# Performance work log

Measured on AMD Instinct MI355X. Metric: run time of the kernel, lower is better.

## Reference

```python
import jax, jax.numpy as jnp
import numpy as np
import math

DIM = 512
N_HEADS = 8
N_KV_HEADS = 4
HEAD_DIM = DIM // N_HEADS
N_REP = N_HEADS // N_KV_HEADS


def setup_inputs() -> dict:
    key = jax.random.key(0)
    ks = jax.random.split(key, 6)
    B, S = 4, 8192
    x = jax.random.normal(ks[0], (B, S, DIM), dtype=jnp.float32)
    g = jnp.ones((DIM,), dtype=jnp.float32)
    sc = 1.0 / math.sqrt(DIM)
    wq = jax.random.normal(ks[1], (DIM, DIM), dtype=jnp.float32) * sc
    wk = jax.random.normal(ks[2], (N_KV_HEADS * HEAD_DIM, DIM), dtype=jnp.float32) * sc
    wv = jax.random.normal(ks[3], (N_KV_HEADS * HEAD_DIM, DIM), dtype=jnp.float32) * sc
    wo = jax.random.normal(ks[4], (DIM, DIM), dtype=jnp.float32) * sc
    return {"x": x, "g": g, "wq": wq, "wk": wk, "wv": wv, "wo": wo}


def _rmsnorm(x, g, eps=1e-6):
    var = jnp.mean(jnp.square(x), axis=-1, keepdims=True)
    return x * jax.lax.rsqrt(var + eps) * g


def _phi(x):
    # F.elu(x).clamp(min=-0.99) + 1
    return jnp.maximum(jax.nn.elu(x), -0.99) + 1.0


def reference(x, g, wq, wk, wv, wo):
    B, S, _ = x.shape
    h = _rmsnorm(x, g)
    scale = 1.0 / math.sqrt(HEAD_DIM)
    q = (h @ wq.T).reshape(B, S, N_HEADS, HEAD_DIM) * scale          # bshd
    k = (h @ wk.T).reshape(B, S, N_KV_HEADS, HEAD_DIM) * scale       # bsgd
    v = (h @ wv.T).reshape(B, S, N_KV_HEADS, HEAD_DIM)
    # GQA: repeat kv heads to n_heads
    k = jnp.repeat(k, N_REP, axis=2)  # (B,S,H,D)
    v = jnp.repeat(v, N_REP, axis=2)
    q = q.transpose(0, 2, 1, 3)  # (B,H,S,D)
    k = k.transpose(0, 2, 1, 3)
    v = v.transpose(0, 2, 1, 3)
    Q = _phi(q)
    K = _phi(k)
    KV = jnp.sum(K * v, axis=2)       # (B,H,D)  elementwise-product sum over s
    K_sum = jnp.sum(K, axis=2)        # (B,H,D)
    Z = jnp.einsum('bhsd,bhd->bhs', Q, K_sum)[..., None]  # (B,H,S,1)
    Y = Q * KV[:, :, None, :]         # (B,H,S,D)
    Y = Y / (Z + 1e-6)
    Y = Y.transpose(0, 2, 1, 3).reshape(B, S, N_HEADS * HEAD_DIM)
    return Y @ wo.T
```

## Files before the change

### kernel.cpp

```cpp
#include <hip/hip_runtime.h>
#include <math.h>

#define DIM 512
#define SEQ 8192
#define BATCH 4
#define RTOT (BATCH*SEQ)
#define SCALE 0.125f

typedef unsigned short ushort_t;
typedef __attribute__((ext_vector_type(8))) short short8;
typedef __attribute__((ext_vector_type(4))) float float4v;

#define AS1(p) ((__attribute__((address_space(1))) void*)(p))
#define AS3(p) ((__attribute__((address_space(3))) void*)(p))

__device__ __forceinline__ float phi_f(float x){
    return x > 0.f ? x + 1.f : fmaxf(expf(x), 0.01f);
}

__device__ __forceinline__ unsigned short f2bf(float f){
    unsigned int u = __float_as_uint(f);
    u += 0x7fffu + ((u >> 16) & 1u);
    return (unsigned short)(u >> 16);
}

#define WS_NEED 68689920ull

__global__ __launch_bounds__(256) void k_rmsh(const float* __restrict__ x, const float* __restrict__ g,
                                              float* __restrict__ wsf, ushort_t* __restrict__ hb){
    const int t = threadIdx.x, w = t>>6, L = t&63;
    const int row = blockIdx.x*4 + w;
    const float4* xr = (const float4*)(x + (size_t)row*DIM);
    float4 a = xr[L*2], c = xr[L*2+1];
    float s = a.x*a.x+a.y*a.y+a.z*a.z+a.w*a.w
            + c.x*c.x+c.y*c.y+c.z*c.z+c.w*c.w;
    #pragma unroll
    for(int off=1; off<64; off<<=1) s += __shfl_xor(s, off, 64);
    const float rf = rsqrtf(s*(1.0f/DIM) + 1e-6f);
    const float4* gr = (const float4*)g;
    float4 ga = gr[L*2], gb = gr[L*2+1];
    uint4 p;
    p.x = (unsigned)f2bf(a.x*ga.x*rf) | ((unsigned)f2bf(a.y*ga.y*rf)<<16);
    p.y = (unsigned)f2bf(a.z*ga.z*rf) | ((unsigned)f2bf(a.w*ga.w*rf)<<16);
    p.z = (unsigned)f2bf(c.x*gb.x*rf) | ((unsigned)f2bf(c.y*gb.y*rf)<<16);
    p.w = (unsigned)f2bf(c.z*gb.z*rf) | ((unsigned)f2bf(c.w*gb.w*rf)<<16);
    *(uint4*)(hb + (size_t)row*DIM + L*8) = p;
    if(blockIdx.x==0){
        for(int i=t;i<2048;i+=256) wsf[i]=0.f;
    }
}

__global__ __launch_bounds__(256) void k_wcast(const float* __restrict__ wq, const float* __restrict__ wk,
                                               const float* __restrict__ wv, const float* __restrict__ wo,
                                               ushort_t* __restrict__ wqb, ushort_t* __restrict__ wob,
                                               ushort_t* __restrict__ wkvb){
    const int idx = (blockIdx.x*256 + threadIdx.x)*4;
    const float* src; ushort_t* dst; int di;
    if(idx < 262144){ src = wq + idx; dst = wqb; di = idx; }
    else if(idx < 524288){ di = idx - 262144; src = wo + di; dst = wob; }
    else {
        int f = idx - 524288;
        int g = f >> 16, rem = f & 65535;
        int row = rem >> 9, col = rem & 511;
        src = (row < 64) ? (wk + (size_t)((g<<6)+row)*DIM + col)
                         : (wv + (size_t)((g<<6)+row-64)*DIM + col);
        dst = wkvb; di = f;
    }
    float4 v = *(const float4*)src;
    uint2 p;
    p.x = (unsigned)f2bf(v.x) | ((unsigned)f2bf(v.y)<<16);
    p.y = (unsigned)f2bf(v.z) | ((unsigned)f2bf(v.w)<<16);
    *(uint2*)(dst + di) = p;
}

__global__ __launch_bounds__(256) void k_kv_mfma(const ushort_t* __restrict__ hb,
                                                 const ushort_t* __restrict__ wkvb,
                                                 float* __restrict__ wsf){
    __shared__ ushort_t At[128*32];
    __shared__ ushort_t Bt[128*32];
    const int t = threadIdx.x, w = t>>6, L = t&63;
    const int lr = L&15, q = L>>4;
    const int r0 = blockIdx.x*128, gh = blockIdx.y;
    const int b = r0 >> 13;
    const int c0 = t, c1 = 256+t;
    const ushort_t* gA0 = hb + (size_t)(r0 + (c0>>2))*DIM + (c0&3)*8;
    const ushort_t* gA1 = hb + (size_t)(r0 + (c1>>2))*DIM + (c1&3)*8;
    const ushort_t* wb  = wkvb + (size_t)gh*128*DIM;
    const ushort_t* gB0 = wb + (size_t)(c0>>2)*DIM + (c0&3)*8;
    const ushort_t* gB1 = wb + (size_t)(c1>>2)*DIM + (c1&3)*8;

    float4v acc[2][8];
    #pragma unroll
    for(int i=0;i<2;i++)
        #pragma unroll
        for(int j=0;j<8;j++) acc[i][j] = (float4v){0.f,0.f,0.f,0.f};

    for(int ks=0; ks<16; ks++){
        __syncthreads();
        __builtin_amdgcn_global_load_lds(AS1(gA0), AS3(At + (w*64)*8),       16, 0, 0);
        __builtin_amdgcn_global_load_lds(AS1(gA1), AS3(At + (256 + w*64)*8), 16, 0, 0);
        __builtin_amdgcn_global_load_lds(AS1(gB0), AS3(Bt + (w*64)*8),       16, 0, 0);
        __builtin_amdgcn_global_load_lds(AS1(gB1), AS3(Bt + (256 + w*64)*8), 16, 0, 0);
        gA0 += 32; gA1 += 32; gB0 += 32; gB1 += 32;
        __syncthreads();
        short8 af[2], bf[8];
        #pragma unroll
        for(int mt=0; mt<2; mt++)
            af[mt] = *(const short8*)(At + (w*32 + mt*16 + lr)*32 + q*8);
        #pragma unroll
        for(int nt=0; nt<8; nt++)
            bf[nt] = *(const short8*)(Bt + (nt*16 + lr)*32 + q*8);
        #pragma unroll
        for(int mt=0; mt<2; mt++)
            #pragma unroll
            for(int nt=0; nt<8; nt++)
                acc[mt][nt] = __builtin_amdgcn_mfma_f32_16x16x32_bf16(af[mt], bf[nt], acc[mt][nt], 0,0,0);
    }

    #pragma unroll
    for(int nt=0; nt<4; nt++){
        float skv=0.f, sks=0.f;
        #pragma unroll
        for(int mt=0; mt<2; mt++)
            #pragma unroll
            for(int r=0; r<4; r++){
                float K = phi_f(acc[mt][nt][r]*SCALE);
                skv = fmaf(K, acc[mt][nt+4][r], skv);
                sks += K;
            }
        skv += __shfl_xor(skv,16,64); skv += __shfl_xor(skv,32,64);
        sks += __shfl_xor(sks,16,64); sks += __shfl_xor(sks,32,64);
        if(q==0){
            atomicAdd(&wsf[       b*256 + gh*64 + nt*16 + lr], skv);
            atomicAdd(&wsf[1024 + b*256 + gh*64 + nt*16 + lr], sks);
        }
    }
}

__global__ __launch_bounds__(256) void k_q_mfma(const ushort_t* __restrict__ hb,
                                                const ushort_t* __restrict__ wqb,
                                                const float* __restrict__ wsf,
                                                ushort_t* __restrict__ yb){
    __shared__ ushort_t At[128*32];
    __shared__ ushort_t Bt[128*32];
    __shared__ ushort_t Yt[128*128];
    const int t = threadIdx.x, w = t>>6, L = t&63;
    const int lr = L&15, q = L>>4;
    const int wr = w>>1, wc = w&1;
    const int r0 = blockIdx.x*128, ct = blockIdx.y;
    const int b = r0 >> 13;
    const int c0 = t, c1 = 256+t;
    const ushort_t* gA0 = hb + (size_t)(r0 + (c0>>2))*DIM + (c0&3)*8;
    const ushort_t* gA1 = hb + (size_t)(r0 + (c1>>2))*DIM + (c1&3)*8;
    const ushort_t* wbq = wqb + (size_t)ct*128*DIM;
    const ushort_t* gB0 = wbq + (size_t)(c0>>2)*DIM + (c0&3)*8;
    const ushort_t* gB1 = wbq + (size_t)(c1>>2)*DIM + (c1&3)*8;

    float4v acc[4][4];
    #pragma unroll
    for(int i=0;i<4;i++)
        #pragma unroll
        for(int j=0;j<4;j++) acc[i][j] = (float4v){0.f,0.f,0.f,0.f};

    for(int ks=0; ks<16; ks++){
        __syncthreads();
        __builtin_amdgcn_global_load_lds(AS1(gA0), AS3(At + (w*64)*8),       16, 0, 0);
        __builtin_amdgcn_global_load_lds(AS1(gA1), AS3(At + (256 + w*64)*8), 16, 0, 0);
        __builtin_amdgcn_global_load_lds(AS1(gB0), AS3(Bt + (w*64)*8),       16, 0, 0);
        __builtin_amdgcn_global_load_lds(AS1(gB1), AS3(Bt + (256 + w*64)*8), 16, 0, 0);
        gA0 += 32; gA1 += 32; gB0 += 32; gB1 += 32;
        __syncthreads();
        short8 af[4], bf[4];
        #pragma unroll
        for(int mt=0; mt<4; mt++)
            af[mt] = *(const short8*)(At + (wr*64 + mt*16 + lr)*32 + q*8);
        #pragma unroll
        for(int nt=0; nt<4; nt++)
            bf[nt] = *(const short8*)(Bt + (wc*64 + nt*16 + lr)*32 + q*8);
        #pragma unroll
        for(int mt=0; mt<4; mt++)
            #pragma unroll
            for(int nt=0; nt<4; nt++)
                acc[mt][nt] = __builtin_amdgcn_mfma_f32_16x16x32_bf16(af[mt], bf[nt], acc[mt][nt], 0,0,0);
    }

    float ksf[4], kvf[4];
    #pragma unroll
    for(int nt=0; nt<4; nt++){
        ksf[nt] = wsf[1024 + b*256 + ct*64 + nt*16 + lr];
        kvf[nt] = wsf[       b*256 + ct*64 + nt*16 + lr];
    }
    #pragma unroll
    for(int mt=0; mt<4; mt++)
        #pragma unroll
        for(int nt=0; nt<4; nt++)
            #pragma unroll
            for(int r=0; r<4; r++)
                acc[mt][nt][r] = phi_f(acc[mt][nt][r]*SCALE);
    float zi[4][4];
    #pragma unroll
    for(int mt=0; mt<4; mt++)
        #pragma unroll
        for(int r=0; r<4; r++){
            float zv = acc[mt][0][r]*ksf[0] + acc[mt][1][r]*ksf[1]
                     + acc[mt][2][r]*ksf[2] + acc[mt][3][r]*ksf[3];
            zv += __shfl_xor(zv,1,64); zv += __shfl_xor(zv,2,64);
            zv += __shfl_xor(zv,4,64); zv += __shfl_xor(zv,8,64);
            zi[mt][r] = 1.0f/(zv + 1e-6f);
        }
    #pragma unroll
    for(int mt=0; mt<4; mt++)
        #pragma unroll
        for(int nt=0; nt<4; nt++)
            #pragma unroll
            for(int r=0; r<4; r++)
                Yt[(wr*64 + mt*16 + q*4 + r)*128 + wc*64 + nt*16 + lr]
                    = f2bf(acc[mt][nt][r]*kvf[nt]*zi[mt][r]);
    __syncthreads();
    #pragma unroll
    for(int i=0;i<8;i++){
        int u = (i*256 + t)*8;
        int rr = u>>7, cc = u&127;
        *(uint4*)(yb + (size_t)(r0+rr)*DIM + ct*128 + cc) = *(const uint4*)(Yt + u);
    }
}

__global__ __launch_bounds__(256) void k_out_mfma(const ushort_t* __restrict__ yb,
                                                  const ushort_t* __restrict__ wob,
                                                  float* __restrict__ out){
    __shared__ ushort_t At[128*32];
    __shared__ ushort_t Bt[128*32];
    const int t = threadIdx.x, w = t>>6, L = t&63;
    const int lr = L&15, q = L>>4;
    const int wr = w>>1, wc = w&1;
    const int r0 = blockIdx.x*128, ct = blockIdx.y;
    const int c0 = t, c1 = 256+t;
    const ushort_t* gA0 = yb + (size_t)(r0 + (c0>>2))*DIM + (c0&3)*8;
    const ushort_t* gA1 = yb + (size_t)(r0 + (c1>>2))*DIM + (c1&3)*8;
    const ushort_t* wbo = wob + (size_t)ct*128*DIM;
    const ushort_t* gB0 = wbo + (size_t)(c0>>2)*DIM + (c0&3)*8;
    const ushort_t* gB1 = wbo + (size_t)(c1>>2)*DIM + (c1&3)*8;

    float4v acc[4][4];
    #pragma unroll
    for(int i=0;i<4;i++)
        #pragma unroll
        for(int j=0;j<4;j++) acc[i][j] = (float4v){0.f,0.f,0.f,0.f};

    for(int ks=0; ks<16; ks++){
        __syncthreads();
        __builtin_amdgcn_global_load_lds(AS1(gA0), AS3(At + (w*64)*8),       16, 0, 0);
        __builtin_amdgcn_global_load_lds(AS1(gA1), AS3(At + (256 + w*64)*8), 16, 0, 0);
        __builtin_amdgcn_global_load_lds(AS1(gB0), AS3(Bt + (w*64)*8),       16, 0, 0);
        __builtin_amdgcn_global_load_lds(AS1(gB1), AS3(Bt + (256 + w*64)*8), 16, 0, 0);
        gA0 += 32; gA1 += 32; gB0 += 32; gB1 += 32;
        __syncthreads();
        short8 af[4], bf[4];
        #pragma unroll
        for(int mt=0; mt<4; mt++)
            af[mt] = *(const short8*)(At + (wr*64 + mt*16 + lr)*32 + q*8);
        #pragma unroll
        for(int nt=0; nt<4; nt++)
            bf[nt] = *(const short8*)(Bt + (wc*64 + nt*16 + lr)*32 + q*8);
        #pragma unroll
        for(int mt=0; mt<4; mt++)
            #pragma unroll
            for(int nt=0; nt<4; nt++)
                acc[mt][nt] = __builtin_amdgcn_mfma_f32_16x16x32_bf16(af[mt], bf[nt], acc[mt][nt], 0,0,0);
    }
    #pragma unroll
    for(int mt=0; mt<4; mt++)
        #pragma unroll
        for(int nt=0; nt<4; nt++)
            #pragma unroll
            for(int r=0; r<4; r++)
                out[(size_t)(r0 + wr*64 + mt*16 + q*4 + r)*DIM + ct*128 + wc*64 + nt*16 + lr]
                    = acc[mt][nt][r];
}

#define OFF_KV 0
#define OFF_KS 1024
#define OFF_R  2048

__global__ __launch_bounds__(256) void k_rms_f32(const float* __restrict__ x, float* __restrict__ ws){
    const int row  = blockIdx.x*4 + (threadIdx.x>>6);
    const int lane = threadIdx.x & 63;
    const float4* xr = (const float4*)(x + (size_t)row*DIM);
    float4 a = xr[lane];
    float4 b = xr[lane+64];
    float s = a.x*a.x+a.y*a.y+a.z*a.z+a.w*a.w
            + b.x*b.x+b.y*b.y+b.z*b.z+b.w*b.w;
    #pragma unroll
    for(int off=32; off; off>>=1) s += __shfl_xor(s, off, 64);
    if(lane==0) ws[OFF_R+row] = rsqrtf(s*(1.0f/DIM) + 1e-6f);
    if(blockIdx.x==0){
        for(int i=threadIdx.x;i<2048;i+=256) ws[i]=0.f;
    }
}

__global__ __launch_bounds__(256) void k_kv_f32(const float* __restrict__ x, const float* __restrict__ g,
                                            const float* __restrict__ wk, const float* __restrict__ wv,
                                            float* __restrict__ ws){
    __shared__ float sAT[16][128];
    __shared__ float sB[16][128];
    __shared__ float rl[128];
    __shared__ float red[64][16];
    const int t  = threadIdx.x;
    const int r0 = blockIdx.x * 128;
    const int gh = blockIdx.y;
    const int b  = r0 / SEQ;
    if(t < 128) rl[t] = ws[OFF_R + r0 + t];
    const int ti = t & 15, tj = t >> 4;
    const int ri = ti*4, cj = tj*4;
    const int srow = t & 127;
    const int skk  = (t >> 7) * 8;
    const float* xrow = x + (size_t)(r0 + srow)*DIM + skk;
    const float* wrow = (srow < 64) ? (wk + (size_t)(gh*64 + srow)*DIM + skk)
                                    : (wv + (size_t)(gh*64 + (srow-64))*DIM + skk);
    const float* gp = g + skk;
    float accK[8][4], accV[8][4];
    #pragma unroll
    for(int i=0;i<8;i++)
        #pragma unroll
        for(int j=0;j<4;j++){ accK[i][j]=0.f; accV[i][j]=0.f; }
    __syncthreads();
    const float rr = rl[srow];
    for(int k0=0;k0<DIM;k0+=16){
        float4 xa = *(const float4*)(xrow + k0);
        float4 xb = *(const float4*)(xrow + k0 + 4);
        float4 ga = *(const float4*)(gp + k0);
        float4 gb = *(const float4*)(gp + k0 + 4);
        float4 wa = *(const float4*)(wrow + k0);
        float4 wb = *(const float4*)(wrow + k0 + 4);
        __syncthreads();
        sAT[skk+0][srow]=xa.x*ga.x*rr; sAT[skk+1][srow]=xa.y*ga.y*rr;
        sAT[skk+2][srow]=xa.z*ga.z*rr; sAT[skk+3][srow]=xa.w*ga.w*rr;
        sAT[skk+4][srow]=xb.x*gb.x*rr; sAT[skk+5][srow]=xb.y*gb.y*rr;
        sAT[skk+6][srow]=xb.z*gb.z*rr; sAT[skk+7][srow]=xb.w*gb.w*rr;
        sB[skk+0][srow]=wa.x; sB[skk+1][srow]=wa.y; sB[skk+2][srow]=wa.z; sB[skk+3][srow]=wa.w;
        sB[skk+4][srow]=wb.x; sB[skk+5][srow]=wb.y; sB[skk+6][srow]=wb.z; sB[skk+7][srow]=wb.w;
        __syncthreads();
        #pragma unroll
        for(int kk=0;kk<16;kk++){
            float4 a0 = *(const float4*)&sAT[kk][ri];
            float4 a1 = *(const float4*)&sAT[kk][ri+64];
            float4 bk = *(const float4*)&sB[kk][cj];
            float4 bv = *(const float4*)&sB[kk][cj+64];
            float av[8] = {a0.x,a0.y,a0.z,a0.w,a1.x,a1.y,a1.z,a1.w};
            float bk4[4]= {bk.x,bk.y,bk.z,bk.w};
            float bv4[4]= {bv.x,bv.y,bv.z,bv.w};
            #pragma unroll
            for(int i=0;i<8;i++)
                #pragma unroll
                for(int j=0;j<4;j++){
                    accK[i][j] = fmaf(av[i], bk4[j], accK[i][j]);
                    accV[i][j] = fmaf(av[i], bv4[j], accV[i][j]);
                }
        }
    }
    float pKV[4], pKs[4];
    #pragma unroll
    for(int j=0;j<4;j++){
        float skv=0.f, sks=0.f;
        #pragma unroll
        for(int i=0;i<8;i++){
            float kvv = phi_f(accK[i][j]*SCALE);
            skv = fmaf(kvv, accV[i][j], skv);
            sks += kvv;
        }
        pKV[j]=skv; pKs[j]=sks;
    }
    __syncthreads();
    #pragma unroll
    for(int j=0;j<4;j++) red[cj+j][ti] = pKV[j];
    __syncthreads();
    if(t<64){
        float s2=0.f;
        for(int i=0;i<16;i++) s2 += red[t][i];
        atomicAdd(&ws[OFF_KV + b*256 + gh*64 + t], s2);
    }
    __syncthreads();
    #pragma unroll
    for(int j=0;j<4;j++) red[cj+j][ti] = pKs[j];
    __syncthreads();
    if(t<64){
        float s2=0.f;
        for(int i=0;i<16;i++) s2 += red[t][i];
        atomicAdd(&ws[OFF_KS + b*256 + gh*64 + t], s2);
    }
}

__global__ __launch_bounds__(256) void k_qo_f32(const float* __restrict__ x, const float* __restrict__ g,
                                            const float* __restrict__ wq, const float* __restrict__ wo,
                                            const float* __restrict__ ws, float* __restrict__ out){
    __shared__ float qT[512][32];
    __shared__ float sAT[16][32];
    __shared__ float sB[16][128];
    __shared__ float rl[32];
    __shared__ float KVl[256];
    __shared__ float Ksl[256];
    __shared__ float zb[256];
    const int t  = threadIdx.x;
    const int r0 = blockIdx.x * 32;
    const int b  = r0 / SEQ;
    if(t<32) rl[t] = ws[OFF_R + r0 + t];
    KVl[t] = ws[OFF_KV + b*256 + t];
    Ksl[t] = ws[OFF_KS + b*256 + t];
    const int ti = t & 7, tj = t >> 3;
    const int ri = ti*4, cj = tj*4;
    const int srow = t & 31, skk = (t>>5)*2;
    const int sj = t & 127, skkB = (t>>7)*8;
    const float* xrow = x + (size_t)(r0+srow)*DIM + skk;
    const float* gp = g + skk;
    __syncthreads();
    const float rr = rl[srow];
    for(int ct=0; ct<4; ct++){
        const float* wqb = wq + (size_t)(ct*128 + sj)*DIM + skkB;
        float acc[4][4];
        #pragma unroll
        for(int i=0;i<4;i++)
            #pragma unroll
            for(int j=0;j<4;j++) acc[i][j]=0.f;
        for(int k0=0;k0<DIM;k0+=16){
            float2 xa = *(const float2*)(xrow + k0);
            float2 ga = *(const float2*)(gp + k0);
            float4 wa = *(const float4*)(wqb + k0);
            float4 wb2= *(const float4*)(wqb + k0 + 4);
            __syncthreads();
            sAT[skk+0][srow] = xa.x*ga.x*rr;
            sAT[skk+1][srow] = xa.y*ga.y*rr;
            sB[skkB+0][sj]=wa.x; sB[skkB+1][sj]=wa.y; sB[skkB+2][sj]=wa.z; sB[skkB+3][sj]=wa.w;
            sB[skkB+4][sj]=wb2.x; sB[skkB+5][sj]=wb2.y; sB[skkB+6][sj]=wb2.z; sB[skkB+7][sj]=wb2.w;
            __syncthreads();
            #pragma unroll
            for(int kk=0;kk<16;kk++){
                float4 a = *(const float4*)&sAT[kk][ri];
                float4 bb= *(const float4*)&sB[kk][cj];
                float av[4]={a.x,a.y,a.z,a.w};
                float bv[4]={bb.x,bb.y,bb.z,bb.w};
                #pragma unroll
                for(int i=0;i<4;i++)
                    #pragma unroll
                    for(int j=0;j<4;j++)
                        acc[i][j] = fmaf(av[i], bv[j], acc[i][j]);
            }
        }
        #pragma unroll
        for(int i=0;i<4;i++)
            #pragma unroll
            for(int j=0;j<4;j++)
                qT[ct*128+cj+j][ri+i] = phi_f(acc[i][j]*SCALE);
    }
    __syncthreads();
    {
        const int row = t>>3, h = t&7;
        const float* ks = &Ksl[(h>>1)*64];
        float z = 0.f;
        #pragma unroll
        for(int d=0;d<64;d++) z = fmaf(qT[h*64+d][row], ks[d], z);
        zb[row*8+h] = 1.0f/(z + 1e-6f);
    }
    __syncthreads();
    #pragma unroll 4
    for(int i2=0;i2<64;i2++){
        int f = i2*256 + t;
        int col = f>>5, row = f&31;
        int h = col>>6;
        float kvv = KVl[((h>>1)<<6) + (col&63)];
        qT[col][row] *= kvv * zb[row*8+h];
    }
    __syncthreads();
    for(int ct=0;ct<4;ct++){
        const float* wob = wo + (size_t)(ct*128 + sj)*DIM + skkB;
        float acc[4][4];
        #pragma unroll
        for(int i=0;i<4;i++)
            #pragma unroll
            for(int j=0;j<4;j++) acc[i][j]=0.f;
        for(int k0=0;k0<DIM;k0+=16){
            float4 wa = *(const float4*)(wob + k0);
            float4 wb2= *(const float4*)(wob + k0 + 4);
            __syncthreads();
            sB[skkB+0][sj]=wa.x; sB[skkB+1][sj]=wa.y; sB[skkB+2][sj]=wa.z; sB[skkB+3][sj]=wa.w;
            sB[skkB+4][sj]=wb2.x; sB[skkB+5][sj]=wb2.y; sB[skkB+6][sj]=wb2.z; sB[skkB+7][sj]=wb2.w;
            __syncthreads();
            #pragma unroll
            for(int kk=0;kk<16;kk++){
                float4 a = *(const float4*)&qT[k0+kk][ri];
                float4 bb= *(const float4*)&sB[kk][cj];
                float av[4]={a.x,a.y,a.z,a.w};
                float bv[4]={bb.x,bb.y,bb.z,bb.w};
                #pragma unroll
                for(int i=0;i<4;i++)
                    #pragma unroll
                    for(int j=0;j<4;j++)
                        acc[i][j] = fmaf(av[i], bv[j], acc[i][j]);
            }
        }
        #pragma unroll
        for(int i=0;i<4;i++){
            float4 st; st.x=acc[i][0]; st.y=acc[i][1]; st.z=acc[i][2]; st.w=acc[i][3];
            *(float4*)(out + (size_t)(r0+ri+i)*DIM + ct*128 + cj) = st;
        }
    }
}

extern "C" void kernel_launch(void* const* d_in, const int* in_sizes, int n_in,
                              void* d_out, int out_size, void* d_ws, size_t ws_size,
                              hipStream_t stream){
    (void)in_sizes; (void)n_in; (void)out_size;
    const float* x  = (const float*)d_in[0];
    const float* g  = (const float*)d_in[1];
    const float* wq = (const float*)d_in[2];
    const float* wk = (const float*)d_in[3];
    const float* wv = (const float*)d_in[4];
    const float* wo = (const float*)d_in[5];
    float* out = (float*)d_out;

    if(ws_size >= WS_NEED){
        float* wsf = (float*)d_ws;
        ushort_t* wqb  = (ushort_t*)((char*)d_ws + 8192);
        ushort_t* wob  = wqb  + 262144;
        ushort_t* wkvb = wob  + 262144;
        ushort_t* hb   = wkvb + 262144;
        ushort_t* yb   = hb   + 16777216;

        hipLaunchKernelGGL(k_rmsh,    dim3(RTOT/4),      dim3(256), 0, stream, x, g, wsf, hb);
        hipLaunchKernelGGL(k_wcast,   dim3(768),         dim3(256), 0, stream, wq, wk, wv, wo, wqb, wob, wkvb);
        hipLaunchKernelGGL(k_kv_mfma, dim3(RTOT/128, 4), dim3(256), 0, stream, hb, wkvb, wsf);
        hipLaunchKernelGGL(k_q_mfma,  dim3(RTOT/128, 4), dim3(256), 0, stream, hb, wqb, wsf, yb);
        hipLaunchKernelGGL(k_out_mfma,dim3(RTOT/128, 4), dim3(256), 0, stream, yb, wob, out);
    } else {
        float* ws = (float*)d_ws;
        hipLaunchKernelGGL(k_rms_f32, dim3(RTOT/4),      dim3(256), 0, stream, x, ws);
        hipLaunchKernelGGL(k_kv_f32,  dim3(RTOT/128, 4), dim3(256), 0, stream, x, g, wk, wv, ws);
        hipLaunchKernelGGL(k_qo_f32,  dim3(RTOT/32),     dim3(256), 0, stream, x, g, wq, wo, ws, out);
    }
}
```

Before: 228.7 us.

## Register-prefetch GEMM tiles two steps ahead and alias LDS in q kernel

Replaces the synchronous global_load_lds staging in the three MFMA GEMM kernels with register-staged loads issued two k-steps ahead, so global latency overlaps the MFMA work. Tiles are written to LDS after each compute step, and the loops are fully unrolled. The q kernel reuses the A/B staging LDS for the Y output tile to shrink its shared memory footprint, and launch bounds now request 2 blocks per SM. The cost is higher register pressure from the extra staging registers plus an occupancy hint that may force spills.

```diff
diff --git a/kernel.cpp b/kernel.cpp
--- a/kernel.cpp
+++ b/kernel.cpp
@@ -10,9 +10,6 @@
 typedef unsigned short ushort_t;
 typedef __attribute__((ext_vector_type(8))) short short8;
 typedef __attribute__((ext_vector_type(4))) float float4v;
-
-#define AS1(p) ((__attribute__((address_space(1))) void*)(p))
-#define AS3(p) ((__attribute__((address_space(3))) void*)(p))
 
 __device__ __forceinline__ float phi_f(float x){
     return x > 0.f ? x + 1.f : fmaxf(expf(x), 0.01f);
@@ -73,9 +70,9 @@
     *(uint2*)(dst + di) = p;
 }
 
-__global__ __launch_bounds__(256) void k_kv_mfma(const ushort_t* __restrict__ hb,
-                                                 const ushort_t* __restrict__ wkvb,
-                                                 float* __restrict__ wsf){
+__global__ __launch_bounds__(256,2) void k_kv_mfma(const ushort_t* __restrict__ hb,
+                                                   const ushort_t* __restrict__ wkvb,
+                                                   float* __restrict__ wsf){
     __shared__ ushort_t At[128*32];
     __shared__ ushort_t Bt[128*32];
     const int t = threadIdx.x, w = t>>6, L = t&63;
@@ -95,14 +92,22 @@
         #pragma unroll
         for(int j=0;j<8;j++) acc[i][j] = (float4v){0.f,0.f,0.f,0.f};
 
+    uint4 sa0[2], sa1[2], sb0[2], sb1[2];
+    sa0[1]=*(const uint4*)gA0; sa1[1]=*(const uint4*)gA1;
+    sb0[1]=*(const uint4*)gB0; sb1[1]=*(const uint4*)gB1;
+    *(uint4*)(At+c0*8)=sa0[1]; *(uint4*)(At+c1*8)=sa1[1];
+    *(uint4*)(Bt+c0*8)=sb0[1]; *(uint4*)(Bt+c1*8)=sb1[1];
+    sa0[0]=*(const uint4*)(gA0+32); sa1[0]=*(const uint4*)(gA1+32);
+    sb0[0]=*(const uint4*)(gB0+32); sb1[0]=*(const uint4*)(gB1+32);
+    __syncthreads();
+
+    #pragma unroll
     for(int ks=0; ks<16; ks++){
-        __syncthreads();
-        __builtin_amdgcn_global_load_lds(AS1(gA0), AS3(At + (w*64)*8),       16, 0, 0);
-        __builtin_amdgcn_global_load_lds(AS1(gA1), AS3(At + (256 + w*64)*8), 16, 0, 0);
-        __builtin_amdgcn_global_load_lds(AS1(gB0), AS3(Bt + (w*64)*8),       16, 0, 0);
-        __builtin_amdgcn_global_load_lds(AS1(gB1), AS3(Bt + (256 + w*64)*8), 16, 0, 0);
-        gA0 += 32; gA1 += 32; gB0 += 32; gB1 += 32;
-        __syncthreads();
+        const int pf = (ks+1)&1, wr_ = ks&1;
+        if(ks<14){
+            sa0[pf]=*(const uint4*)(gA0+(ks+2)*32); sa1[pf]=*(const uint4*)(gA1+(ks+2)*32);
+            sb0[pf]=*(const uint4*)(gB0+(ks+2)*32); sb1[pf]=*(const uint4*)(gB1+(ks+2)*32);
+        }
         short8 af[2], bf[8];
         #pragma unroll
         for(int mt=0; mt<2; mt++)
@@ -115,6 +120,12 @@
             #pragma unroll
             for(int nt=0; nt<8; nt++)
                 acc[mt][nt] = __builtin_amdgcn_mfma_f32_16x16x32_bf16(af[mt], bf[nt], acc[mt][nt], 0,0,0);
+        __syncthreads();
+        if(ks<15){
+            *(uint4*)(At+c0*8)=sa0[wr_]; *(uint4*)(At+c1*8)=sa1[wr_];
+            *(uint4*)(Bt+c0*8)=sb0[wr_]; *(uint4*)(Bt+c1*8)=sb1[wr_];
+            __syncthreads();
+        }
     }
 
     #pragma unroll
@@ -137,13 +148,13 @@
     }
 }
 
-__global__ __launch_bounds__(256) void k_q_mfma(const ushort_t* __restrict__ hb,
-                                                const ushort_t* __restrict__ wqb,
-                                                const float* __restrict__ wsf,
-                                                ushort_t* __restrict__ yb){
-    __shared__ ushort_t At[128*32];
-    __shared__ ushort_t Bt[128*32];
-    __shared__ ushort_t Yt[128*128];
+__global__ __launch_bounds__(256,2) void k_q_mfma(const ushort_t* __restrict__ hb,
+                                                  const ushort_t* __restrict__ wqb,
+                                                  const float* __restrict__ wsf,
+                                                  ushort_t* __restrict__ yb){
+    __shared__ ushort_t smem[128*128];
+    ushort_t* At = smem;
+    ushort_t* Bt = smem + 4096;
     const int t = threadIdx.x, w = t>>6, L = t&63;
     const int lr = L&15, q = L>>4;
     const int wr = w>>1, wc = w&1;
@@ -162,14 +173,22 @@
         #pragma unroll
         for(int j=0;j<4;j++) acc[i][j] = (float4v){0.f,0.f,0.f,0.f};
 
+    uint4 sa0[2], sa1[2], sb0[2], sb1[2];
+    sa0[1]=*(const uint4*)gA0; sa1[1]=*(const uint4*)gA1;
+    sb0[1]=*(const uint4*)gB0; sb1[1]=*(const uint4*)gB1;
+    *(uint4*)(At+c0*8)=sa0[1]; *(uint4*)(At+c1*8)=sa1[1];
+    *(uint4*)(Bt+c0*8)=sb0[1]; *(uint4*)(Bt+c1*8)=sb1[1];
+    sa0[0]=*(const uint4*)(gA0+32); sa1[0]=*(const uint4*)(gA1+32);
+    sb0[0]=*(const uint4*)(gB0+32); sb1[0]=*(const uint4*)(gB1+32);
+    __syncthreads();
+
+    #pragma unroll
     for(int ks=0; ks<16; ks++){
-        __syncthreads();
-        __builtin_amdgcn_global_load_lds(AS1(gA0), AS3(At + (w*64)*8),       16, 0, 0);
-        __builtin_amdgcn_global_load_lds(AS1(gA1), AS3(At + (256 + w*64)*8), 16, 0, 0);
-        __builtin_amdgcn_global_load_lds(AS1(gB0), AS3(Bt + (w*64)*8),       16, 0, 0);
-        __builtin_amdgcn_global_load_lds(AS1(gB1), AS3(Bt + (256 + w*64)*8), 16, 0, 0);
-        gA0 += 32; gA1 += 32; gB0 += 32; gB1 += 32;
-        __syncthreads();
+        const int pf = (ks+1)&1, wr_ = ks&1;
+        if(ks<14){
+            sa0[pf]=*(const uint4*)(gA0+(ks+2)*32); sa1[pf]=*(const uint4*)(gA1+(ks+2)*32);
+            sb0[pf]=*(const uint4*)(gB0+(ks+2)*32); sb1[pf]=*(const uint4*)(gB1+(ks+2)*32);
+        }
         short8 af[4], bf[4];
         #pragma unroll
         for(int mt=0; mt<4; mt++)
@@ -182,6 +201,12 @@
             #pragma unroll
             for(int nt=0; nt<4; nt++)
                 acc[mt][nt] = __builtin_amdgcn_mfma_f32_16x16x32_bf16(af[mt], bf[nt], acc[mt][nt], 0,0,0);
+        __syncthreads();
+        if(ks<15){
+            *(uint4*)(At+c0*8)=sa0[wr_]; *(uint4*)(At+c1*8)=sa1[wr_];
+            *(uint4*)(Bt+c0*8)=sb0[wr_]; *(uint4*)(Bt+c1*8)=sb1[wr_];
+            __syncthreads();
+        }
     }
 
     float ksf[4], kvf[4];
@@ -208,6 +233,7 @@
             zv += __shfl_xor(zv,4,64); zv += __shfl_xor(zv,8,64);
             zi[mt][r] = 1.0f/(zv + 1e-6f);
         }
+    ushort_t* Yt = smem;
     #pragma unroll
     for(int mt=0; mt<4; mt++)
         #pragma unroll
@@ -225,9 +251,9 @@
     }
 }
 
-__global__ __launch_bounds__(256) void k_out_mfma(const ushort_t* __restrict__ yb,
-                                                  const ushort_t* __restrict__ wob,
-                                                  float* __restrict__ out){
+__global__ __launch_bounds__(256,2) void k_out_mfma(const ushort_t* __restrict__ yb,
+                                                    const ushort_t* __restrict__ wob,
+                                                    float* __restrict__ out){
     __shared__ ushort_t At[128*32];
     __shared__ ushort_t Bt[128*32];
     const int t = threadIdx.x, w = t>>6, L = t&63;
@@ -247,14 +273,22 @@
         #pragma unroll
         for(int j=0;j<4;j++) acc[i][j] = (float4v){0.f,0.f,0.f,0.f};
 
+    uint4 sa0[2], sa1[2], sb0[2], sb1[2];
+    sa0[1]=*(const uint4*)gA0; sa1[1]=*(const uint4*)gA1;
+    sb0[1]=*(const uint4*)gB0; sb1[1]=*(const uint4*)gB1;
+    *(uint4*)(At+c0*8)=sa0[1]; *(uint4*)(At+c1*8)=sa1[1];
+    *(uint4*)(Bt+c0*8)=sb0[1]; *(uint4*)(Bt+c1*8)=sb1[1];
+    sa0[0]=*(const uint4*)(gA0+32); sa1[0]=*(const uint4*)(gA1+32);
+    sb0[0]=*(const uint4*)(gB0+32); sb1[0]=*(const uint4*)(gB1+32);
+    __syncthreads();
+
+    #pragma unroll
     for(int ks=0; ks<16; ks++){
-        __syncthreads();
-        __builtin_amdgcn_global_load_lds(AS1(gA0), AS3(At + (w*64)*8),       16, 0, 0);
-        __builtin_amdgcn_global_load_lds(AS1(gA1), AS3(At + (256 + w*64)*8), 16, 0, 0);
-        __builtin_amdgcn_global_load_lds(AS1(gB0), AS3(Bt + (w*64)*8),       16, 0, 0);
-        __builtin_amdgcn_global_load_lds(AS1(gB1), AS3(Bt + (256 + w*64)*8), 16, 0, 0);
-        gA0 += 32; gA1 += 32; gB0 += 32; gB1 += 32;
-        __syncthreads();
+        const int pf = (ks+1)&1, wr_ = ks&1;
+        if(ks<14){
+            sa0[pf]=*(const uint4*)(gA0+(ks+2)*32); sa1[pf]=*(const uint4*)(gA1+(ks+2)*32);
+            sb0[pf]=*(const uint4*)(gB0+(ks+2)*32); sb1[pf]=*(const uint4*)(gB1+(ks+2)*32);
+        }
         short8 af[4], bf[4];
         #pragma unroll
         for(int mt=0; mt<4; mt++)
@@ -267,6 +301,12 @@
             #pragma unroll
             for(int nt=0; nt<4; nt++)
                 acc[mt][nt] = __builtin_amdgcn_mfma_f32_16x16x32_bf16(af[mt], bf[nt], acc[mt][nt], 0,0,0);
+        __syncthreads();
+        if(ks<15){
+            *(uint4*)(At+c0*8)=sa0[wr_]; *(uint4*)(At+c1*8)=sa1[wr_];
+            *(uint4*)(Bt+c0*8)=sb0[wr_]; *(uint4*)(Bt+c1*8)=sb1[wr_];
+            __syncthreads();
+        }
     }
     #pragma unroll
     for(int mt=0; mt<4; mt++)
```

After: 408.7 us. +78.7%, slower.

## Fuse Q projection, linear attention and output GEMM into one row-block kernel

Applied to the files above, without the earlier changes.

Merges the Q GEMM, phi/normalisation epilogue and output projection into a single kernel that keeps the 64-row h tile and the bf16 Y tile in shared memory, so the Y intermediate is no longer written to and read back from global memory. The KV kernel is restructured the same way: the full 64x512 A tile is staged once into LDS, and weight fragments are read directly from global memory per wave instead of being double-synchronised into LDS each k-step. This cuts global traffic and barriers and shrinks workspace, at the cost of large per-thread accumulator arrays (4x8 tiles), 64KB LDS per block and uncached direct weight loads. Occupancy is limited by the launch bound of two blocks.

```diff
diff --git a/kernel.cpp b/kernel.cpp
--- a/kernel.cpp
+++ b/kernel.cpp
@@ -11,9 +11,6 @@
 typedef __attribute__((ext_vector_type(8))) short short8;
 typedef __attribute__((ext_vector_type(4))) float float4v;
 
-#define AS1(p) ((__attribute__((address_space(1))) void*)(p))
-#define AS3(p) ((__attribute__((address_space(3))) void*)(p))
-
 __device__ __forceinline__ float phi_f(float x){
     return x > 0.f ? x + 1.f : fmaxf(expf(x), 0.01f);
 }
@@ -24,7 +21,7 @@
     return (unsigned short)(u >> 16);
 }
 
-#define WS_NEED 68689920ull
+#define WS_NEED 35135488ull
 
 __global__ __launch_bounds__(256) void k_rmsh(const float* __restrict__ x, const float* __restrict__ g,
                                               float* __restrict__ wsf, ushort_t* __restrict__ hb){
@@ -73,47 +70,52 @@
     *(uint2*)(dst + di) = p;
 }
 
-__global__ __launch_bounds__(256) void k_kv_mfma(const ushort_t* __restrict__ hb,
-                                                 const ushort_t* __restrict__ wkvb,
-                                                 float* __restrict__ wsf){
-    __shared__ ushort_t At[128*32];
-    __shared__ ushort_t Bt[128*32];
+__device__ __forceinline__ void stage_A(const ushort_t* __restrict__ src, size_t r0,
+                                        ushort_t* As, int w, int L){
+    #pragma unroll
+    for(int i=0;i<16;i++){
+        const int row = i*4 + w;
+        uint4 v = *(const uint4*)(src + (size_t)(r0+row)*DIM + L*8);
+        *(uint4*)(&As[(L>>2)*2048 + row*32 + (L&3)*8]) = v;
+    }
+}
+
+__global__ __launch_bounds__(256,2) void k_kv2(const ushort_t* __restrict__ hb,
+                                               const ushort_t* __restrict__ wkvb,
+                                               float* __restrict__ wsf){
+    __shared__ ushort_t As[32768];
     const int t = threadIdx.x, w = t>>6, L = t&63;
     const int lr = L&15, q = L>>4;
-    const int r0 = blockIdx.x*128, gh = blockIdx.y;
-    const int b = r0 >> 13;
-    const int c0 = t, c1 = 256+t;
-    const ushort_t* gA0 = hb + (size_t)(r0 + (c0>>2))*DIM + (c0&3)*8;
-    const ushort_t* gA1 = hb + (size_t)(r0 + (c1>>2))*DIM + (c1&3)*8;
-    const ushort_t* wb  = wkvb + (size_t)gh*128*DIM;
-    const ushort_t* gB0 = wb + (size_t)(c0>>2)*DIM + (c0&3)*8;
-    const ushort_t* gB1 = wb + (size_t)(c1>>2)*DIM + (c1&3)*8;
-
-    float4v acc[2][8];
-    #pragma unroll
-    for(int i=0;i<2;i++)
+    const size_t r0 = (size_t)blockIdx.x*64;
+    const int b = (int)(r0 >> 13);
+
+    stage_A(hb, r0, As, w, L);
+    __syncthreads();
+
+    const ushort_t* bp[8];
+    #pragma unroll
+    for(int nt=0;nt<8;nt++)
+        bp[nt] = wkvb + ((size_t)w*128 + nt*16 + lr)*DIM + q*8;
+
+    float4v acc[4][8];
+    #pragma unroll
+    for(int i=0;i<4;i++)
         #pragma unroll
         for(int j=0;j<8;j++) acc[i][j] = (float4v){0.f,0.f,0.f,0.f};
 
+    #pragma unroll
     for(int ks=0; ks<16; ks++){
-        __syncthreads();
-        __builtin_amdgcn_global_load_lds(AS1(gA0), AS3(At + (w*64)*8),       16, 0, 0);
-        __builtin_amdgcn_global_load_lds(AS1(gA1), AS3(At + (256 + w*64)*8), 16, 0, 0);
-        __builtin_amdgcn_global_load_lds(AS1(gB0), AS3(Bt + (w*64)*8),       16, 0, 0);
-        __builtin_amdgcn_global_load_lds(AS1(gB1), AS3(Bt + (256 + w*64)*8), 16, 0, 0);
-        gA0 += 32; gA1 += 32; gB0 += 32; gB1 += 32;
-        __syncthreads();
-        short8 af[2], bf[8];
-        #pragma unroll
-        for(int mt=0; mt<2; mt++)
-            af[mt] = *(const short8*)(At + (w*32 + mt*16 + lr)*32 + q*8);
-        #pragma unroll
-        for(int nt=0; nt<8; nt++)
-            bf[nt] = *(const short8*)(Bt + (nt*16 + lr)*32 + q*8);
-        #pragma unroll
-        for(int mt=0; mt<2; mt++)
-            #pragma unroll
-            for(int nt=0; nt<8; nt++)
+        short8 bf[8];
+        #pragma unroll
+        for(int nt=0;nt<8;nt++) bf[nt] = *(const short8*)(bp[nt] + ks*32);
+        short8 af[4];
+        #pragma unroll
+        for(int mt=0;mt<4;mt++)
+            af[mt] = *(const short8*)(As + ks*2048 + (mt*16+lr)*32 + q*8);
+        #pragma unroll
+        for(int mt=0;mt<4;mt++)
+            #pragma unroll
+            for(int nt=0;nt<8;nt++)
                 acc[mt][nt] = __builtin_amdgcn_mfma_f32_16x16x32_bf16(af[mt], bf[nt], acc[mt][nt], 0,0,0);
     }
 
@@ -121,7 +123,7 @@
     for(int nt=0; nt<4; nt++){
         float skv=0.f, sks=0.f;
         #pragma unroll
-        for(int mt=0; mt<2; mt++)
+        for(int mt=0; mt<4; mt++)
             #pragma unroll
             for(int r=0; r<4; r++){
                 float K = phi_f(acc[mt][nt][r]*SCALE);
@@ -131,151 +133,129 @@
         skv += __shfl_xor(skv,16,64); skv += __shfl_xor(skv,32,64);
         sks += __shfl_xor(sks,16,64); sks += __shfl_xor(sks,32,64);
         if(q==0){
-            atomicAdd(&wsf[       b*256 + gh*64 + nt*16 + lr], skv);
-            atomicAdd(&wsf[1024 + b*256 + gh*64 + nt*16 + lr], sks);
-        }
-    }
-}
-
-__global__ __launch_bounds__(256) void k_q_mfma(const ushort_t* __restrict__ hb,
+            atomicAdd(&wsf[       b*256 + w*64 + nt*16 + lr], skv);
+            atomicAdd(&wsf[1024 + b*256 + w*64 + nt*16 + lr], sks);
+        }
+    }
+}
+
+__global__ __launch_bounds__(256,2) void k_qout(const ushort_t* __restrict__ hb,
                                                 const ushort_t* __restrict__ wqb,
+                                                const ushort_t* __restrict__ wob,
                                                 const float* __restrict__ wsf,
-                                                ushort_t* __restrict__ yb){
-    __shared__ ushort_t At[128*32];
-    __shared__ ushort_t Bt[128*32];
-    __shared__ ushort_t Yt[128*128];
+                                                float* __restrict__ out){
+    __shared__ ushort_t As[32768];
     const int t = threadIdx.x, w = t>>6, L = t&63;
     const int lr = L&15, q = L>>4;
-    const int wr = w>>1, wc = w&1;
-    const int r0 = blockIdx.x*128, ct = blockIdx.y;
-    const int b = r0 >> 13;
-    const int c0 = t, c1 = 256+t;
-    const ushort_t* gA0 = hb + (size_t)(r0 + (c0>>2))*DIM + (c0&3)*8;
-    const ushort_t* gA1 = hb + (size_t)(r0 + (c1>>2))*DIM + (c1&3)*8;
-    const ushort_t* wbq = wqb + (size_t)ct*128*DIM;
-    const ushort_t* gB0 = wbq + (size_t)(c0>>2)*DIM + (c0&3)*8;
-    const ushort_t* gB1 = wbq + (size_t)(c1>>2)*DIM + (c1&3)*8;
-
-    float4v acc[4][4];
+    const size_t r0 = (size_t)blockIdx.x*64;
+    const int b = (int)(r0 >> 13);
+
+    stage_A(hb, r0, As, w, L);
+    __syncthreads();
+
+    float4v acc[4][8];
     #pragma unroll
     for(int i=0;i<4;i++)
         #pragma unroll
-        for(int j=0;j<4;j++) acc[i][j] = (float4v){0.f,0.f,0.f,0.f};
-
-    for(int ks=0; ks<16; ks++){
-        __syncthreads();
-        __builtin_amdgcn_global_load_lds(AS1(gA0), AS3(At + (w*64)*8),       16, 0, 0);
-        __builtin_amdgcn_global_load_lds(AS1(gA1), AS3(At + (256 + w*64)*8), 16, 0, 0);
-        __builtin_amdgcn_global_load_lds(AS1(gB0), AS3(Bt + (w*64)*8),       16, 0, 0);
-        __builtin_amdgcn_global_load_lds(AS1(gB1), AS3(Bt + (256 + w*64)*8), 16, 0, 0);
-        gA0 += 32; gA1 += 32; gB0 += 32; gB1 += 32;
-        __syncthreads();
-        short8 af[4], bf[4];
-        #pragma unroll
-        for(int mt=0; mt<4; mt++)
-            af[mt] = *(const short8*)(At + (wr*64 + mt*16 + lr)*32 + q*8);
-        #pragma unroll
-        for(int nt=0; nt<4; nt++)
-            bf[nt] = *(const short8*)(Bt + (wc*64 + nt*16 + lr)*32 + q*8);
-        #pragma unroll
-        for(int mt=0; mt<4; mt++)
-            #pragma unroll
-            for(int nt=0; nt<4; nt++)
-                acc[mt][nt] = __builtin_amdgcn_mfma_f32_16x16x32_bf16(af[mt], bf[nt], acc[mt][nt], 0,0,0);
-    }
-
-    float ksf[4], kvf[4];
-    #pragma unroll
-    for(int nt=0; nt<4; nt++){
-        ksf[nt] = wsf[1024 + b*256 + ct*64 + nt*16 + lr];
-        kvf[nt] = wsf[       b*256 + ct*64 + nt*16 + lr];
-    }
-    #pragma unroll
-    for(int mt=0; mt<4; mt++)
-        #pragma unroll
-        for(int nt=0; nt<4; nt++)
-            #pragma unroll
-            for(int r=0; r<4; r++)
+        for(int j=0;j<8;j++) acc[i][j] = (float4v){0.f,0.f,0.f,0.f};
+
+    {
+        const ushort_t* bp[8];
+        #pragma unroll
+        for(int nt=0;nt<8;nt++)
+            bp[nt] = wqb + ((size_t)w*128 + nt*16 + lr)*DIM + q*8;
+        #pragma unroll
+        for(int ks=0; ks<16; ks++){
+            short8 bf[8];
+            #pragma unroll
+            for(int nt=0;nt<8;nt++) bf[nt] = *(const short8*)(bp[nt] + ks*32);
+            short8 af[4];
+            #pragma unroll
+            for(int mt=0;mt<4;mt++)
+                af[mt] = *(const short8*)(As + ks*2048 + (mt*16+lr)*32 + q*8);
+            #pragma unroll
+            for(int mt=0;mt<4;mt++)
+                #pragma unroll
+                for(int nt=0;nt<8;nt++)
+                    acc[mt][nt] = __builtin_amdgcn_mfma_f32_16x16x32_bf16(af[mt], bf[nt], acc[mt][nt], 0,0,0);
+        }
+    }
+
+    float ksf[8], kvf[8];
+    #pragma unroll
+    for(int nt=0;nt<8;nt++){
+        const int d = (nt&3)*16 + lr;
+        kvf[nt] = wsf[       b*256 + w*64 + d];
+        ksf[nt] = wsf[1024 + b*256 + w*64 + d];
+    }
+    #pragma unroll
+    for(int mt=0;mt<4;mt++)
+        #pragma unroll
+        for(int nt=0;nt<8;nt++)
+            #pragma unroll
+            for(int r=0;r<4;r++)
                 acc[mt][nt][r] = phi_f(acc[mt][nt][r]*SCALE);
-    float zi[4][4];
-    #pragma unroll
-    for(int mt=0; mt<4; mt++)
-        #pragma unroll
-        for(int r=0; r<4; r++){
-            float zv = acc[mt][0][r]*ksf[0] + acc[mt][1][r]*ksf[1]
+    float zi0[4][4], zi1[4][4];
+    #pragma unroll
+    for(int mt=0;mt<4;mt++)
+        #pragma unroll
+        for(int r=0;r<4;r++){
+            float z0 = acc[mt][0][r]*ksf[0] + acc[mt][1][r]*ksf[1]
                      + acc[mt][2][r]*ksf[2] + acc[mt][3][r]*ksf[3];
-            zv += __shfl_xor(zv,1,64); zv += __shfl_xor(zv,2,64);
-            zv += __shfl_xor(zv,4,64); zv += __shfl_xor(zv,8,64);
-            zi[mt][r] = 1.0f/(zv + 1e-6f);
-        }
-    #pragma unroll
-    for(int mt=0; mt<4; mt++)
-        #pragma unroll
-        for(int nt=0; nt<4; nt++)
-            #pragma unroll
-            for(int r=0; r<4; r++)
-                Yt[(wr*64 + mt*16 + q*4 + r)*128 + wc*64 + nt*16 + lr]
-                    = f2bf(acc[mt][nt][r]*kvf[nt]*zi[mt][r]);
-    __syncthreads();
-    #pragma unroll
-    for(int i=0;i<8;i++){
-        int u = (i*256 + t)*8;
-        int rr = u>>7, cc = u&127;
-        *(uint4*)(yb + (size_t)(r0+rr)*DIM + ct*128 + cc) = *(const uint4*)(Yt + u);
-    }
-}
-
-__global__ __launch_bounds__(256) void k_out_mfma(const ushort_t* __restrict__ yb,
-                                                  const ushort_t* __restrict__ wob,
-                                                  float* __restrict__ out){
-    __shared__ ushort_t At[128*32];
-    __shared__ ushort_t Bt[128*32];
-    const int t = threadIdx.x, w = t>>6, L = t&63;
-    const int lr = L&15, q = L>>4;
-    const int wr = w>>1, wc = w&1;
-    const int r0 = blockIdx.x*128, ct = blockIdx.y;
-    const int c0 = t, c1 = 256+t;
-    const ushort_t* gA0 = yb + (size_t)(r0 + (c0>>2))*DIM + (c0&3)*8;
-    const ushort_t* gA1 = yb + (size_t)(r0 + (c1>>2))*DIM + (c1&3)*8;
-    const ushort_t* wbo = wob + (size_t)ct*128*DIM;
-    const ushort_t* gB0 = wbo + (size_t)(c0>>2)*DIM + (c0&3)*8;
-    const ushort_t* gB1 = wbo + (size_t)(c1>>2)*DIM + (c1&3)*8;
-
-    float4v acc[4][4];
+            float z1 = acc[mt][4][r]*ksf[4] + acc[mt][5][r]*ksf[5]
+                     + acc[mt][6][r]*ksf[6] + acc[mt][7][r]*ksf[7];
+            z0 += __shfl_xor(z0,1,64); z0 += __shfl_xor(z0,2,64);
+            z0 += __shfl_xor(z0,4,64); z0 += __shfl_xor(z0,8,64);
+            z1 += __shfl_xor(z1,1,64); z1 += __shfl_xor(z1,2,64);
+            z1 += __shfl_xor(z1,4,64); z1 += __shfl_xor(z1,8,64);
+            zi0[mt][r] = 1.0f/(z0 + 1e-6f);
+            zi1[mt][r] = 1.0f/(z1 + 1e-6f);
+        }
+    __syncthreads();
+    #pragma unroll
+    for(int mt=0;mt<4;mt++)
+        #pragma unroll
+        for(int nt=0;nt<8;nt++)
+            #pragma unroll
+            for(int r=0;r<4;r++){
+                float zi = (nt<4) ? zi0[mt][r] : zi1[mt][r];
+                float y = acc[mt][nt][r]*kvf[nt]*zi;
+                As[(w*4 + (nt>>1))*2048 + (mt*16 + q*4 + r)*32 + (nt&1)*16 + lr] = f2bf(y);
+            }
+    __syncthreads();
+
     #pragma unroll
     for(int i=0;i<4;i++)
         #pragma unroll
-        for(int j=0;j<4;j++) acc[i][j] = (float4v){0.f,0.f,0.f,0.f};
-
-    for(int ks=0; ks<16; ks++){
-        __syncthreads();
-        __builtin_amdgcn_global_load_lds(AS1(gA0), AS3(At + (w*64)*8),       16, 0, 0);
-        __builtin_amdgcn_global_load_lds(AS1(gA1), AS3(At + (256 + w*64)*8), 16, 0, 0);
-        __builtin_amdgcn_global_load_lds(AS1(gB0), AS3(Bt + (w*64)*8),       16, 0, 0);
-        __builtin_amdgcn_global_load_lds(AS1(gB1), AS3(Bt + (256 + w*64)*8), 16, 0, 0);
-        gA0 += 32; gA1 += 32; gB0 += 32; gB1 += 32;
-        __syncthreads();
-        short8 af[4], bf[4];
-        #pragma unroll
-        for(int mt=0; mt<4; mt++)
-            af[mt] = *(const short8*)(At + (wr*64 + mt*16 + lr)*32 + q*8);
-        #pragma unroll
-        for(int nt=0; nt<4; nt++)
-            bf[nt] = *(const short8*)(Bt + (wc*64 + nt*16 + lr)*32 + q*8);
-        #pragma unroll
-        for(int mt=0; mt<4; mt++)
-            #pragma unroll
-            for(int nt=0; nt<4; nt++)
-                acc[mt][nt] = __builtin_amdgcn_mfma_f32_16x16x32_bf16(af[mt], bf[nt], acc[mt][nt], 0,0,0);
-    }
-    #pragma unroll
-    for(int mt=0; mt<4; mt++)
-        #pragma unroll
-        for(int nt=0; nt<4; nt++)
-            #pragma unroll
-            for(int r=0; r<4; r++)
-                out[(size_t)(r0 + wr*64 + mt*16 + q*4 + r)*DIM + ct*128 + wc*64 + nt*16 + lr]
-                    = acc[mt][nt][r];
+        for(int j=0;j<8;j++) acc[i][j] = (float4v){0.f,0.f,0.f,0.f};
+    {
+        const ushort_t* bp[8];
+        #pragma unroll
+        for(int nt=0;nt<8;nt++)
+            bp[nt] = wob + ((size_t)w*128 + nt*16 + lr)*DIM + q*8;
+        #pragma unroll
+        for(int ks=0; ks<16; ks++){
+            short8 bf[8];
+            #pragma unroll
+            for(int nt=0;nt<8;nt++) bf[nt] = *(const short8*)(bp[nt] + ks*32);
+            short8 af[4];
+            #pragma unroll
+            for(int mt=0;mt<4;mt++)
+                af[mt] = *(const short8*)(As + ks*2048 + (mt*16+lr)*32 + q*8);
+            #pragma unroll
+            for(int mt=0;mt<4;mt++)
+                #pragma unroll
+                for(int nt=0;nt<8;nt++)
+                    acc[mt][nt] = __builtin_amdgcn_mfma_f32_16x16x32_bf16(af[mt], bf[nt], acc[mt][nt], 0,0,0);
+        }
+    }
+    #pragma unroll
+    for(int mt=0;mt<4;mt++)
+        #pragma unroll
+        for(int nt=0;nt<8;nt++)
+            #pragma unroll
+            for(int r=0;r<4;r++)
+                out[(r0 + mt*16 + q*4 + r)*DIM + w*128 + nt*16 + lr] = acc[mt][nt][r];
 }
 
 #define OFF_KV 0
@@ -523,13 +503,11 @@
         ushort_t* wob  = wqb  + 262144;
         ushort_t* wkvb = wob  + 262144;
         ushort_t* hb   = wkvb + 262144;
-        ushort_t* yb   = hb   + 16777216;
-
-        hipLaunchKernelGGL(k_rmsh,    dim3(RTOT/4),      dim3(256), 0, stream, x, g, wsf, hb);
-        hipLaunchKernelGGL(k_wcast,   dim3(768),         dim3(256), 0, stream, wq, wk, wv, wo, wqb, wob, wkvb);
-        hipLaunchKernelGGL(k_kv_mfma, dim3(RTOT/128, 4), dim3(256), 0, stream, hb, wkvb, wsf);
-        hipLaunchKernelGGL(k_q_mfma,  dim3(RTOT/128, 4), dim3(256), 0, stream, hb, wqb, wsf, yb);
-        hipLaunchKernelGGL(k_out_mfma,dim3(RTOT/128, 4), dim3(256), 0, stream, yb, wob, out);
+
+        hipLaunchKernelGGL(k_rmsh,  dim3(RTOT/4),  dim3(256), 0, stream, x, g, wsf, hb);
+        hipLaunchKernelGGL(k_wcast, dim3(768),     dim3(256), 0, stream, wq, wk, wv, wo, wqb, wob, wkvb);
+        hipLaunchKernelGGL(k_kv2,   dim3(RTOT/64), dim3(256), 0, stream, hb, wkvb, wsf);
+        hipLaunchKernelGGL(k_qout,  dim3(RTOT/64), dim3(256), 0, stream, hb, wqb, wob, wsf, out);
     } else {
         float* ws = (float*)d_ws;
         hipLaunchKernelGGL(k_rms_f32, dim3(RTOT/4),      dim3(256), 0, stream, x, ws);
```

Result: slower. 240.8 us (+5.3%).
